# Performance work log

Hardware: AMD Instinct MI355X
Metric: run time of the kernel (lower is better)

Reference implementation:

```python
import jax, jax.numpy as jnp
import numpy as np

L, B, D, H = 2048, 2, 1024, 16
DK = D // H
SCALE = DK ** -0.5


def setup_inputs() -> dict:
    key = jax.random.key(0)
    ks = jax.random.split(key, 11)
    w_std = D ** -0.5
    return {
        "query": jax.random.normal(ks[0], (L, B, D), dtype=jnp.float32),
        "key": jax.random.normal(ks[1], (L, B, D), dtype=jnp.float32),
        "value": jax.random.normal(ks[2], (L, B, D), dtype=jnp.float32),
        "WQ_w": jax.random.normal(ks[3], (D, D), dtype=jnp.float32) * w_std,
        "WQ_b": jnp.zeros((D,), dtype=jnp.float32),
        "WK_w": jax.random.normal(ks[4], (D, D), dtype=jnp.float32) * w_std,
        "WK_b": jnp.zeros((D,), dtype=jnp.float32),
        "WV_w": jax.random.normal(ks[5], (D, D), dtype=jnp.float32) * w_std,
        "WV_b": jnp.zeros((D,), dtype=jnp.float32),
        "WO_w": jax.random.normal(ks[6], (D, D), dtype=jnp.float32) * w_std,
        "WO_b": jnp.zeros((D,), dtype=jnp.float32),
    }


def reference(query, key, value, WQ_w, WQ_b, WK_w, WK_b, WV_w, WV_b, WO_w, WO_b):
    tgt_len, batch, _ = query.shape
    src_len = key.shape[0]
    # linear projections (torch Linear: x @ W^T + b)
    q = (query @ WQ_w.T + WQ_b) * SCALE            # [L, B, D]
    k = key @ WK_w.T + WK_b                        # [S, B, D]
    v = value @ WV_w.T + WV_b                      # [S, B, D]
    # split heads: [len, B, D] -> [B*H, len, DK]
    q = q.reshape(tgt_len, batch * H, DK).transpose(1, 0, 2)
    k = k.reshape(src_len, batch * H, DK).transpose(1, 0, 2)
    v = v.reshape(src_len, batch * H, DK).transpose(1, 0, 2)
    # attention scores and softmax (full [B*H, L, S] matrix, as in the original)
    scores = jnp.einsum('nld,nsd->nls', q, k)      # [B*H, L, S]
    probs = jax.nn.softmax(scores, axis=-1)
    out = jnp.einsum('nls,nsd->nld', probs, v)     # [B*H, L, DK]
    # merge heads: [B*H, L, DK] -> [L, B, D]
    out = out.transpose(1, 0, 2).reshape(tgt_len, batch, D)
    return out @ WO_w.T + WO_b
```

## Files before the change

### kernel.cpp

```cpp
#include <hip/hip_runtime.h>
#include <hip/hip_fp16.h>

#define LL 2048
#define BB 2
#define DD 1024
#define HH 16
#define DKK 64

typedef _Float16 h8 __attribute__((ext_vector_type(8)));
typedef _Float16 h4 __attribute__((ext_vector_type(4)));
typedef float f4 __attribute__((ext_vector_type(4)));
typedef float f16v __attribute__((ext_vector_type(16)));

#define BAR() do {                                              \
    asm volatile("s_waitcnt lgkmcnt(0)" ::: "memory");          \
    __builtin_amdgcn_s_barrier();                               \
    asm volatile("" ::: "memory");                              \
} while (0)

__device__ __forceinline__ void gload_lds16(const void* g, void* l) {
    __builtin_amdgcn_global_load_lds(
        (const __attribute__((address_space(1))) void*)g,
        (__attribute__((address_space(3))) void*)l, 16, 0, 0);
}

__device__ __forceinline__ unsigned pack2h(float a, float b) {
    union { _Float16 h[2]; unsigned u; } x;
    x.h[0] = (_Float16)a; x.h[1] = (_Float16)b;
    return x.u;
}

__global__ __launch_bounds__(256) void cvt_all(
    const float* __restrict__ x0, const float* __restrict__ x1,
    const float* __restrict__ x2, const float* __restrict__ w0,
    const float* __restrict__ w1, const float* __restrict__ w2,
    const float* __restrict__ w3,
    _Float16* __restrict__ y0, _Float16* __restrict__ y1,
    _Float16* __restrict__ y2, _Float16* __restrict__ z0,
    _Float16* __restrict__ z1, _Float16* __restrict__ z2,
    _Float16* __restrict__ z3)
{
    const int sel = blockIdx.y;
    if (sel >= 3 && blockIdx.x >= 512) return;
    const float* src = (sel == 0) ? x0 : (sel == 1) ? x1 : (sel == 2) ? x2
                     : (sel == 3) ? w0 : (sel == 4) ? w1 : (sel == 5) ? w2 : w3;
    _Float16* dst = (sel == 0) ? y0 : (sel == 1) ? y1 : (sel == 2) ? y2
                  : (sel == 3) ? z0 : (sel == 4) ? z1 : (sel == 5) ? z2 : z3;
    const int i = (blockIdx.x * 256 + threadIdx.x) * 8;
    f4 a = *(const f4*)(src + i);
    f4 b = *(const f4*)(src + i + 4);
    h8 o = {(_Float16)a.x, (_Float16)a.y, (_Float16)a.z, (_Float16)a.w,
            (_Float16)b.x, (_Float16)b.y, (_Float16)b.z, (_Float16)b.w};
    *(h8*)(dst + i) = o;
}

__global__ __launch_bounds__(256) void qkv_proj(
    const _Float16* __restrict__ xq, const _Float16* __restrict__ xk,
    const _Float16* __restrict__ xv,
    const _Float16* __restrict__ wq, const float* __restrict__ bq,
    const _Float16* __restrict__ wk, const float* __restrict__ bk,
    const _Float16* __restrict__ wv, const float* __restrict__ bv,
    _Float16* __restrict__ qh, _Float16* __restrict__ kh,
    _Float16* __restrict__ vth)
{
    const int mode = blockIdx.z;
    const _Float16* X    = (mode == 0) ? xq : (mode == 1) ? xk : xv;
    const _Float16* W    = (mode == 0) ? wq : (mode == 1) ? wk : wv;
    const float*    bias = (mode == 0) ? bq : (mode == 1) ? bk : bv;

    __shared__ alignas(16) _Float16 a_sm[128 * 32];
    __shared__ alignas(16) _Float16 b_sm[128 * 32];

    const int tid  = threadIdx.x;
    const int lane = tid & 63;
    const int wave = tid >> 6;
    const int wm = (wave & 1) * 64;
    const int wn = (wave >> 1) * 64;
    const int m0 = blockIdx.x * 128;
    const int n0 = blockIdx.y * 128;

    const int srow = tid >> 2;
    const int scol = (tid & 3) * 8;
    const int lds_base = wave * 512;

    f4 acc[4][4];
    #pragma unroll
    for (int i = 0; i < 4; i++)
        #pragma unroll
        for (int j = 0; j < 4; j++)
            #pragma unroll
            for (int r = 0; r < 4; r++) acc[i][j][r] = 0.f;

    const int fr = lane & 15;
    const int fk = (lane >> 4) * 8;

    for (int k0 = 0; k0 < DD; k0 += 32) {
        gload_lds16(X + (size_t)(m0 + srow) * DD + k0 + scol,       &a_sm[lds_base]);
        gload_lds16(X + (size_t)(m0 + 64 + srow) * DD + k0 + scol,  &a_sm[2048 + lds_base]);
        gload_lds16(W + (size_t)(n0 + srow) * DD + k0 + scol,       &b_sm[lds_base]);
        gload_lds16(W + (size_t)(n0 + 64 + srow) * DD + k0 + scol,  &b_sm[2048 + lds_base]);
        __syncthreads();
        h8 af[4], bfr[4];
        #pragma unroll
        for (int i = 0; i < 4; i++) af[i]  = *(const h8*)&a_sm[(wm + i * 16 + fr) * 32 + fk];
        #pragma unroll
        for (int j = 0; j < 4; j++) bfr[j] = *(const h8*)&b_sm[(wn + j * 16 + fr) * 32 + fk];
        #pragma unroll
        for (int i = 0; i < 4; i++)
            #pragma unroll
            for (int j = 0; j < 4; j++)
                acc[i][j] = __builtin_amdgcn_mfma_f32_16x16x32_f16(af[i], bfr[j], acc[i][j], 0, 0, 0);
        __syncthreads();
    }

    const int colc = lane & 15;
    const int rowb = (lane >> 4) * 4;
    #pragma unroll
    for (int i = 0; i < 4; i++) {
        #pragma unroll
        for (int j = 0; j < 4; j++) {
            const int nn = n0 + wn + j * 16 + colc;
            const float bval = bias[nn];
            #pragma unroll
            for (int reg = 0; reg < 4; reg++) {
                const int mm = m0 + wm + i * 16 + rowb + reg;
                float v = acc[i][j][reg] + bval;
                const int b = mm & 1, l = mm >> 1;
                const int h = nn >> 6, dk = nn & 63;
                const int head = b * HH + h;
                if (mode == 0) {
                    v *= 0.1803368801111243f;
                    qh[((size_t)head * LL + l) * DKK + dk] = (_Float16)v;
                } else if (mode == 1) {
                    kh[((size_t)head * LL + l) * DKK + dk] = (_Float16)v;
                } else {
                    vth[((size_t)head * DKK + dk) * LL + l] = (_Float16)v;
                }
            }
        }
    }
}

__global__ __launch_bounds__(512, 4) void attn(
    const _Float16* __restrict__ qh, const _Float16* __restrict__ kh,
    const _Float16* __restrict__ vth, _Float16* __restrict__ oh)
{
    const int rb = blockIdx.y * 16 + blockIdx.x;
    const int lb = (rb & 7) * 64 + (rb >> 3);
    const int head = lb >> 4;
    const int q0   = (lb & 15) * 128;

    const int tid = threadIdx.x, lane = tid & 63, wave = tid >> 6;
    const int qstrip = wave & 3;
    const int sh     = wave >> 2;
    const int qw = q0 + qstrip * 32;

    __shared__ alignas(16) char smem_raw[128 * 72 * 2 + 64 * 136 * 2 + 4 * 32 * 4];
    _Float16 (*k_sm)[72]   = (_Float16(*)[72])smem_raw;
    _Float16 (*vt_sm)[136] = (_Float16(*)[136])(smem_raw + 18432);
    float    (*ls_sm)[32]  = (float(*)[32])(smem_raw + 18432 + 17408);
    float*   xch           = (float*)smem_raw;

    const int rq = lane & 31;
    const int hi = lane >> 5;
    const int kb = hi * 8;
    const int tid8 = tid * 8;

    const _Float16* khead  = kh  + (size_t)head * LL * DKK;
    const _Float16* vthead = vth + (size_t)head * DKK * LL;

    const _Float16* qbase = qh + ((size_t)head * LL + qw + rq) * DKK;
    h8 qa[4];
    #pragma unroll
    for (int kf = 0; kf < 4; kf++) qa[kf] = *(const h8*)(qbase + kf * 16 + kb);

    f16v o0, o1;
    #pragma unroll
    for (int r = 0; r < 16; r++) { o0[r] = 0.f; o1[r] = 0.f; }
    float lsum = 0.f;

    #pragma unroll
    for (int t = 0; t < 2; t++) {
        const int flat = t * 4096 + tid8;
        *(h8*)&k_sm[flat >> 6][flat & 63] = *(const h8*)(khead + flat);
        *(h8*)&vt_sm[flat >> 7][flat & 127] =
            *(const h8*)(vthead + (size_t)(flat >> 7) * LL + (flat & 127));
    }
    BAR();

    for (int it = 0; it < 16; ++it) {
        const int s1 = it * 128 + 128;
        const bool more = (s1 < LL);

        h8 kpre[2], vpre[2];
        if (more) {
            const _Float16* kg = khead + (size_t)s1 * DKK;
            #pragma unroll
            for (int t = 0; t < 2; t++) kpre[t] = *(const h8*)(kg + t * 4096 + tid8);
            #pragma unroll
            for (int t = 0; t < 2; t++) {
                const int flat = t * 4096 + tid8;
                vpre[t] = *(const h8*)(vthead + (size_t)(flat >> 7) * LL + s1 + (flat & 127));
            }
        }

        f16v sc[2];
        #pragma unroll
        for (int st2 = 0; st2 < 2; st2++) {
            const int st = sh * 2 + st2;
            #pragma unroll
            for (int r = 0; r < 16; r++) sc[st2][r] = 0.f;
            #pragma unroll
            for (int kf = 0; kf < 4; kf++) {
                h8 kf8 = *(const h8*)&k_sm[st * 32 + rq][kf * 16 + kb];
                sc[st2] = __builtin_amdgcn_mfma_f32_32x32x16_f16(kf8, qa[kf], sc[st2], 0, 0, 0);
            }
        }

        #pragma unroll
        for (int st2 = 0; st2 < 2; st2++) {
            const int st = sh * 2 + st2;
            float p[16];
            #pragma unroll
            for (int r = 0; r < 16; r++) {
                p[r] = __builtin_amdgcn_exp2f(sc[st2][r]);
                lsum += p[r];
            }
            unsigned own[4][2], part[4][2];
            #pragma unroll
            for (int g = 0; g < 4; g++) {
                own[g][0] = pack2h(p[4 * g],     p[4 * g + 1]);
                own[g][1] = pack2h(p[4 * g + 2], p[4 * g + 3]);
                part[g][0] = __shfl_xor(own[g][0], 32, 64);
                part[g][1] = __shfl_xor(own[g][1], 32, 64);
            }
            #pragma unroll
            for (int j = 0; j < 2; j++) {
                union { unsigned u[4]; h8 h; } pa;
                pa.u[0] = hi ? part[2 * j + 1][0] : own[2 * j][0];
                pa.u[1] = hi ? part[2 * j + 1][1] : own[2 * j][1];
                pa.u[2] = hi ? own[2 * j + 1][0]  : part[2 * j][0];
                pa.u[3] = hi ? own[2 * j + 1][1]  : part[2 * j][1];
                h8 b0 = *(const h8*)&vt_sm[rq][st * 32 + j * 16 + kb];
                h8 b1 = *(const h8*)&vt_sm[32 + rq][st * 32 + j * 16 + kb];
                o0 = __builtin_amdgcn_mfma_f32_32x32x16_f16(pa.h, b0, o0, 0, 0, 0);
                o1 = __builtin_amdgcn_mfma_f32_32x32x16_f16(pa.h, b1, o1, 0, 0, 0);
            }
        }

        BAR();
        if (more) {
            #pragma unroll
            for (int t = 0; t < 2; t++) {
                const int flat = t * 4096 + tid8;
                *(h8*)&k_sm[flat >> 6][flat & 63] = kpre[t];
            }
            #pragma unroll
            for (int t = 0; t < 2; t++) {
                const int flat = t * 4096 + tid8;
                *(h8*)&vt_sm[flat >> 7][flat & 127] = vpre[t];
            }
            BAR();
        }
    }

    lsum += __shfl_xor(lsum, 32, 64);

    float* myx = xch + ((qstrip * 64 + lane) * 33);
    if (sh) {
        #pragma unroll
        for (int r = 0; r < 16; r++) { myx[r] = o0[r]; myx[16 + r] = o1[r]; }
        myx[32] = lsum;
    }
    BAR();
    if (!sh) {
        #pragma unroll
        for (int r = 0; r < 16; r++) { o0[r] += myx[r]; o1[r] += myx[16 + r]; }
        lsum += myx[32];
        ls_sm[wave][rq] = 1.0f / lsum;
        asm volatile("s_waitcnt lgkmcnt(0)" ::: "memory");

        const int b = head >> 4, h = head & 15;
        #pragma unroll
        for (int r = 0; r < 16; r++) {
            const int qrow = (r & 3) + 8 * (r >> 2) + 4 * hi;
            const float inv = ls_sm[wave][qrow];
            const int ql = qw + qrow;
            const size_t base = (size_t)(ql * BB + b) * DD + h * DKK;
            oh[base + rq]      = (_Float16)(o0[r] * inv);
            oh[base + 32 + rq] = (_Float16)(o1[r] * inv);
        }
    }
}

__global__ __launch_bounds__(256) void out_proj(
    const _Float16* __restrict__ oh, const _Float16* __restrict__ wo,
    const float* __restrict__ bo, float* __restrict__ out)
{
    __shared__ alignas(16) _Float16 a_sm[64 * 32];
    __shared__ alignas(16) _Float16 b_sm[128 * 32];
    const int tid = threadIdx.x, lane = tid & 63, wave = tid >> 6;
    const int wm = (wave & 1) * 32, wn = (wave >> 1) * 64;
    const int m0 = blockIdx.x * 64, n0 = blockIdx.y * 128;

    const int srow = tid >> 2;
    const int scol = (tid & 3) * 8;
    const int lds_base = wave * 512;

    f4 acc[2][4];
    #pragma unroll
    for (int i = 0; i < 2; i++)
        #pragma unroll
        for (int j = 0; j < 4; j++)
            #pragma unroll
            for (int r = 0; r < 4; r++) acc[i][j][r] = 0.f;

    const int fr = lane & 15;
    const int fk = (lane >> 4) * 8;

    for (int k0 = 0; k0 < DD; k0 += 32) {
        gload_lds16(oh + (size_t)(m0 + srow) * DD + k0 + scol,      &a_sm[lds_base]);
        gload_lds16(wo + (size_t)(n0 + srow) * DD + k0 + scol,      &b_sm[lds_base]);
        gload_lds16(wo + (size_t)(n0 + 64 + srow) * DD + k0 + scol, &b_sm[2048 + lds_base]);
        __syncthreads();
        h8 af[2], bfr[4];
        #pragma unroll
        for (int i = 0; i < 2; i++) af[i]  = *(const h8*)&a_sm[(wm + i * 16 + fr) * 32 + fk];
        #pragma unroll
        for (int j = 0; j < 4; j++) bfr[j] = *(const h8*)&b_sm[(wn + j * 16 + fr) * 32 + fk];
        #pragma unroll
        for (int i = 0; i < 2; i++)
            #pragma unroll
            for (int j = 0; j < 4; j++)
                acc[i][j] = __builtin_amdgcn_mfma_f32_16x16x32_f16(af[i], bfr[j], acc[i][j], 0, 0, 0);
        __syncthreads();
    }

    const int colc = lane & 15;
    const int rowb = (lane >> 4) * 4;
    #pragma unroll
    for (int i = 0; i < 2; i++) {
        #pragma unroll
        for (int j = 0; j < 4; j++) {
            const int nn = n0 + wn + j * 16 + colc;
            const float bval = bo[nn];
            #pragma unroll
            for (int reg = 0; reg < 4; reg++) {
                const int mm = m0 + wm + i * 16 + rowb + reg;
                out[(size_t)mm * DD + nn] = acc[i][j][reg] + bval;
            }
        }
    }
}

extern "C" void kernel_launch(void* const* d_in, const int* in_sizes, int n_in,
                              void* d_out, int out_size, void* d_ws, size_t ws_size,
                              hipStream_t stream) {
    const float* qin = (const float*)d_in[0];
    const float* kin = (const float*)d_in[1];
    const float* vin = (const float*)d_in[2];
    const float* wq  = (const float*)d_in[3];
    const float* bq  = (const float*)d_in[4];
    const float* wk  = (const float*)d_in[5];
    const float* bk  = (const float*)d_in[6];
    const float* wv  = (const float*)d_in[7];
    const float* bv  = (const float*)d_in[8];
    const float* wo  = (const float*)d_in[9];
    const float* bo  = (const float*)d_in[10];

    const size_t seg = (size_t)32 * LL * DKK;
    _Float16* qh  = (_Float16*)d_ws;
    _Float16* kh  = qh + seg;
    _Float16* vth = kh + seg;
    _Float16* oh  = vth + seg;
    _Float16* wqh = oh + seg;
    _Float16* wkh = wqh + (size_t)DD * DD;
    _Float16* wvh = wkh + (size_t)DD * DD;
    _Float16* woh = wvh + (size_t)DD * DD;
    _Float16* xqh = woh + (size_t)DD * DD;
    _Float16* xkh = xqh + seg;
    _Float16* xvh = xkh + seg;

    hipLaunchKernelGGL(cvt_all, dim3(2048, 7), dim3(256), 0, stream,
                       qin, kin, vin, wq, wk, wv, wo,
                       xqh, xkh, xvh, wqh, wkh, wvh, woh);
    hipLaunchKernelGGL(qkv_proj, dim3(32, 8, 3), dim3(256), 0, stream,
                       xqh, xkh, xvh, wqh, bq, wkh, bk, wvh, bv, qh, kh, vth);
    hipLaunchKernelGGL(attn, dim3(16, 32), dim3(512), 0, stream, qh, kh, vth, oh);
    hipLaunchKernelGGL(out_proj, dim3(64, 8), dim3(256), 0, stream, oh, woh,
                       bo, (float*)d_out);
}
```

Baseline: 225.9 us.

## Double-buffer K/V tiles via direct global-to-LDS loads with XOR swizzle

Result: faster. 219.0 us (-3.1%).

```diff
diff --git a/kernel.cpp b/kernel.cpp
--- a/kernel.cpp
+++ b/kernel.cpp
@@ -155,20 +155,36 @@
     const int sh     = wave >> 2;
     const int qw = q0 + qstrip * 32;
 
-    __shared__ alignas(16) char smem_raw[128 * 72 * 2 + 64 * 136 * 2 + 4 * 32 * 4];
-    _Float16 (*k_sm)[72]   = (_Float16(*)[72])smem_raw;
-    _Float16 (*vt_sm)[136] = (_Float16(*)[136])(smem_raw + 18432);
-    float    (*ls_sm)[32]  = (float(*)[32])(smem_raw + 18432 + 17408);
-    float*   xch           = (float*)smem_raw;
+    __shared__ alignas(16) char smem[65536];
 
     const int rq = lane & 31;
     const int hi = lane >> 5;
     const int kb = hi * 8;
-    const int tid8 = tid * 8;
+    const unsigned key = (unsigned)(rq & 7);
 
     const _Float16* khead  = kh  + (size_t)head * LL * DKK;
     const _Float16* vthead = vth + (size_t)head * DKK * LL;
 
+    const int seg0 = wave * 2;
+    auto stage = [&](int s0, unsigned koff, unsigned voff) {
+        #pragma unroll
+        for (int t = 0; t < 2; t++) {
+            const int i = (seg0 + t) * 64 + lane;
+            const int r = i >> 3, p = i & 7;
+            gload_lds16(khead + (size_t)(s0 + r) * DKK + ((p ^ (r & 7)) << 3),
+                        smem + koff + (unsigned)(seg0 + t) * 1024u);
+        }
+        #pragma unroll
+        for (int t = 0; t < 2; t++) {
+            const int i = (seg0 + t) * 64 + lane;
+            const int r = i >> 4, p = i & 15;
+            gload_lds16(vthead + (size_t)r * LL + s0 + ((p ^ (r & 7)) << 3),
+                        smem + voff + (unsigned)(seg0 + t) * 1024u);
+        }
+    };
+
+    stage(0, 0u, 16384u);
+
     const _Float16* qbase = qh + ((size_t)head * LL + qw + rq) * DKK;
     h8 qa[4];
     #pragma unroll
@@ -179,30 +195,16 @@
     for (int r = 0; r < 16; r++) { o0[r] = 0.f; o1[r] = 0.f; }
     float lsum = 0.f;
 
-    #pragma unroll
-    for (int t = 0; t < 2; t++) {
-        const int flat = t * 4096 + tid8;
-        *(h8*)&k_sm[flat >> 6][flat & 63] = *(const h8*)(khead + flat);
-        *(h8*)&vt_sm[flat >> 7][flat & 127] =
-            *(const h8*)(vthead + (size_t)(flat >> 7) * LL + (flat & 127));
-    }
+    asm volatile("s_waitcnt vmcnt(0)" ::: "memory");
     BAR();
 
     for (int it = 0; it < 16; ++it) {
-        const int s1 = it * 128 + 128;
-        const bool more = (s1 < LL);
-
-        h8 kpre[2], vpre[2];
-        if (more) {
-            const _Float16* kg = khead + (size_t)s1 * DKK;
-            #pragma unroll
-            for (int t = 0; t < 2; t++) kpre[t] = *(const h8*)(kg + t * 4096 + tid8);
-            #pragma unroll
-            for (int t = 0; t < 2; t++) {
-                const int flat = t * 4096 + tid8;
-                vpre[t] = *(const h8*)(vthead + (size_t)(flat >> 7) * LL + s1 + (flat & 127));
-            }
-        }
+        const unsigned cb = (unsigned)(it & 1) * 32768u;
+        const unsigned nb = (unsigned)((it + 1) & 1) * 32768u;
+        if (it < 15) stage((it + 1) * 128, nb, nb + 16384u);
+
+        const char* kc = smem + cb;
+        const char* vc = smem + cb + 16384u;
 
         f16v sc[2];
         #pragma unroll
@@ -212,7 +214,9 @@
             for (int r = 0; r < 16; r++) sc[st2][r] = 0.f;
             #pragma unroll
             for (int kf = 0; kf < 4; kf++) {
-                h8 kf8 = *(const h8*)&k_sm[st * 32 + rq][kf * 16 + kb];
+                h8 kf8 = *(const h8*)(kc +
+                    ((((unsigned)(st * 32 + rq) << 3) +
+                      (((unsigned)(kf * 2 + hi)) ^ key)) << 4));
                 sc[st2] = __builtin_amdgcn_mfma_f32_32x32x16_f16(kf8, qa[kf], sc[st2], 0, 0, 0);
             }
         }
@@ -226,46 +230,39 @@
                 p[r] = __builtin_amdgcn_exp2f(sc[st2][r]);
                 lsum += p[r];
             }
-            unsigned own[4][2], part[4][2];
+            unsigned w0[4], w1[4];
             #pragma unroll
             for (int g = 0; g < 4; g++) {
-                own[g][0] = pack2h(p[4 * g],     p[4 * g + 1]);
-                own[g][1] = pack2h(p[4 * g + 2], p[4 * g + 3]);
-                part[g][0] = __shfl_xor(own[g][0], 32, 64);
-                part[g][1] = __shfl_xor(own[g][1], 32, 64);
+                w0[g] = pack2h(p[4 * g],     p[4 * g + 1]);
+                w1[g] = pack2h(p[4 * g + 2], p[4 * g + 3]);
             }
             #pragma unroll
             for (int j = 0; j < 2; j++) {
+                unsigned x0 = w0[2 * j], y0 = w0[2 * j + 1];
+                unsigned x1 = w1[2 * j], y1 = w1[2 * j + 1];
+                asm("v_permlane32_swap_b32 %0, %1" : "+v"(x0), "+v"(y0));
+                asm("v_permlane32_swap_b32 %0, %1" : "+v"(x1), "+v"(y1));
                 union { unsigned u[4]; h8 h; } pa;
-                pa.u[0] = hi ? part[2 * j + 1][0] : own[2 * j][0];
-                pa.u[1] = hi ? part[2 * j + 1][1] : own[2 * j][1];
-                pa.u[2] = hi ? own[2 * j + 1][0]  : part[2 * j][0];
-                pa.u[3] = hi ? own[2 * j + 1][1]  : part[2 * j][1];
-                h8 b0 = *(const h8*)&vt_sm[rq][st * 32 + j * 16 + kb];
-                h8 b1 = *(const h8*)&vt_sm[32 + rq][st * 32 + j * 16 + kb];
+                pa.u[0] = x0; pa.u[1] = x1; pa.u[2] = y0; pa.u[3] = y1;
+                h8 b0 = *(const h8*)(vc +
+                    ((((unsigned)rq << 4) +
+                      (((unsigned)(st * 4 + j * 2 + hi)) ^ key)) << 4));
+                h8 b1 = *(const h8*)(vc +
+                    ((((unsigned)(32 + rq) << 4) +
+                      (((unsigned)(st * 4 + j * 2 + hi)) ^ key)) << 4));
                 o0 = __builtin_amdgcn_mfma_f32_32x32x16_f16(pa.h, b0, o0, 0, 0, 0);
                 o1 = __builtin_amdgcn_mfma_f32_32x32x16_f16(pa.h, b1, o1, 0, 0, 0);
             }
         }
 
+        asm volatile("s_waitcnt vmcnt(0)" ::: "memory");
         BAR();
-        if (more) {
-            #pragma unroll
-            for (int t = 0; t < 2; t++) {
-                const int flat = t * 4096 + tid8;
-                *(h8*)&k_sm[flat >> 6][flat & 63] = kpre[t];
-            }
-            #pragma unroll
-            for (int t = 0; t < 2; t++) {
-                const int flat = t * 4096 + tid8;
-                *(h8*)&vt_sm[flat >> 7][flat & 127] = vpre[t];
-            }
-            BAR();
-        }
     }
 
     lsum += __shfl_xor(lsum, 32, 64);
 
+    float* xch = (float*)smem;
+    float* lsp = (float*)(smem + 40960);
     float* myx = xch + ((qstrip * 64 + lane) * 33);
     if (sh) {
         #pragma unroll
@@ -277,14 +274,14 @@
         #pragma unroll
         for (int r = 0; r < 16; r++) { o0[r] += myx[r]; o1[r] += myx[16 + r]; }
         lsum += myx[32];
-        ls_sm[wave][rq] = 1.0f / lsum;
+        lsp[qstrip * 32 + rq] = 1.0f / lsum;
         asm volatile("s_waitcnt lgkmcnt(0)" ::: "memory");
 
         const int b = head >> 4, h = head & 15;
         #pragma unroll
         for (int r = 0; r < 16; r++) {
             const int qrow = (r & 3) + 8 * (r >> 2) + 4 * hi;
-            const float inv = ls_sm[wave][qrow];
+            const float inv = lsp[qstrip * 32 + qrow];
             const int ql = qw + qrow;
             const size_t base = (size_t)(ql * BB + b) * DD + h * DKK;
             oh[base + rq]      = (_Float16)(o0[r] * inv);
```
